# Performance work log

Measured on AMD Instinct MI355X. Metric: run time of the kernel, lower is better.

## Reference

```python
import jax, jax.numpy as jnp
import numpy as np

N_NODES = 50000
N_EDGES = 1600000
D = 64          # n_atom_basis = n_filters
NB = 25         # n_basis (RBF)
L = 3           # n_interactions
CUTOFF = 5.0
MAX_Z = 100


def swish(x):
    return x * jax.nn.sigmoid(x)


def setup_inputs() -> dict:
    key = jax.random.key(0)
    ks = jax.random.split(key, 20)
    z = jax.random.randint(ks[0], (N_NODES,), 0, MAX_Z)
    src = jax.random.randint(ks[1], (N_EDGES,), 0, N_NODES)
    dst = jax.random.randint(ks[2], (N_EDGES,), 0, N_NODES)
    rij = jax.random.uniform(ks[3], (N_EDGES,), jnp.float32, 0.3, CUTOFF)
    s = 1.0 / np.sqrt(D)
    emb = jax.random.normal(ks[4], (MAX_Z, D), jnp.float32) * 0.1
    emb = emb.at[0].set(0.0)  # padding_idx=0
    Win = jax.random.normal(ks[5], (L, D, D), jnp.float32) * s
    Wf1 = jax.random.normal(ks[6], (L, NB, D), jnp.float32) * (1.0 / np.sqrt(NB))
    bf1 = jnp.zeros((L, D), jnp.float32)
    Wf2 = jax.random.normal(ks[7], (L, D, D), jnp.float32) * s
    bf2 = jnp.zeros((L, D), jnp.float32)
    Wo1 = jax.random.normal(ks[8], (L, D, D), jnp.float32) * s
    bo1 = jnp.zeros((L, D), jnp.float32)
    Wo2 = jax.random.normal(ks[9], (L, D, D), jnp.float32) * s
    bo2 = jnp.zeros((L, D), jnp.float32)
    gn_alpha = jnp.ones((L, D), jnp.float32)
    gn_gamma = jnp.ones((L, D), jnp.float32)
    gn_beta = jnp.zeros((L, D), jnp.float32)
    return dict(z=z, src=src, dst=dst, rij=rij, emb=emb, Win=Win,
                Wf1=Wf1, bf1=bf1, Wf2=Wf2, bf2=bf2,
                Wo1=Wo1, bo1=bo1, Wo2=Wo2, bo2=bo2,
                gn_alpha=gn_alpha, gn_gamma=gn_gamma, gn_beta=gn_beta)


def reference(z, src, dst, rij, emb, Win, Wf1, bf1, Wf2, bf2,
              Wo1, bo1, Wo2, bo2, gn_alpha, gn_gamma, gn_beta):
    n = z.shape[0]
    # GaussianSmearing(0, cutoff, n_basis)
    offsets = jnp.linspace(0.0, CUTOFF, NB)
    width = offsets[1] - offsets[0]
    coeff = -0.5 / (width * width)
    fij = jnp.exp(coeff * (rij[:, None] - offsets[None, :]) ** 2)  # [E, NB]
    # CosineCutoff
    C = 0.5 * (jnp.cos(rij * (np.pi / CUTOFF)) + 1.0) * (rij < CUTOFF)  # [E]

    feat = emb[z]  # [N, D]
    for l in range(L):
        # cfconv: in2f (no bias), filter MLP gated by cutoff, gather*W, scatter-sum
        x1 = feat @ Win[l]                                            # [N, D]
        W = swish(fij @ Wf1[l] + bf1[l]) @ Wf2[l] + bf2[l]            # [E, D]
        W = W * C[:, None]
        m = x1[src] * W                                               # [E, D]
        agg = jax.ops.segment_sum(m, dst, num_segments=n)             # [N, D]
        # f2out: Dense+swish, Dense; residual
        y = swish(agg @ Wo1[l] + bo1[l]) @ Wo2[l] + bo2[l]
        feat = feat + y
        # GraphNorm over all nodes (single graph)
        mean = feat.mean(axis=0)
        h = feat - gn_alpha[l] * mean
        var = (h * h).mean(axis=0)
        feat = gn_gamma[l] * h * jax.lax.rsqrt(var + 1e-5) + gn_beta[l]

    # softmax readout: per-feature attention over nodes
    w = jax.nn.softmax(feat, axis=0)
    pooled = (w * feat).sum(axis=0)  # [D]
    return feat, pooled
```

## Files before the change

### kernel.cpp

```cpp
#include <hip/hip_runtime.h>
#include <hip/hip_bf16.h>
#include <math.h>

#define D64 64
#define KTAB 4096
#define TROWS (KTAB + 1)
#define CHUNK 8192
#define PARTB 196
#define TABB 387

typedef unsigned int uint4a __attribute__((ext_vector_type(4), aligned(4)));
typedef __attribute__((ext_vector_type(8))) short bf16x8;
typedef __attribute__((ext_vector_type(4))) float f32x4;

__device__ __forceinline__ void atomAddF(float* p, float v) {
  __hip_atomic_fetch_add(p, v, __ATOMIC_RELAXED, __HIP_MEMORY_SCOPE_AGENT);
}
__device__ __forceinline__ float swishf(float x) { return x / (1.0f + expf(-x)); }
__device__ __forceinline__ float bx(unsigned short s) {
  return __uint_as_float((unsigned)s << 16);
}
__device__ __forceinline__ unsigned short f2b(float f) {
  unsigned u = __float_as_uint(f);
  return (unsigned short)((u + 0x7FFFu + ((u >> 16) & 1u)) >> 16);
}

__global__ __launch_bounds__(256) void k_pre(const int* __restrict__ z,
                                             const float* __restrict__ emb,
                                             float* __restrict__ feat,
                                             const float* __restrict__ Win,
                                             const float* __restrict__ Wo1,
                                             const float* __restrict__ Wo2,
                                             unsigned short* __restrict__ Wb,
                                             const int* __restrict__ dst,
                                             int* __restrict__ bcnt,
                                             int total, int nbInit, int E) {
  __shared__ int c[64];
  const int bid = blockIdx.x;
  if (bid < nbInit) {
    int idx = bid * 256 + threadIdx.x;
    if (idx < total) feat[idx] = emb[z[idx >> 6] * D64 + (idx & 63)];
  } else if (bid < nbInit + 18) {
    int idx = (bid - nbInit) * 256 + threadIdx.x;
    if (idx < 3 * 3 * 64 * 8) {
      const int fr = idx & 7;
      const int lane = (idx >> 3) & 63;
      const int m = (idx >> 9) % 3;
      const int l = idx / 1536;
      const int ct = fr >> 1, ks = fr & 1;
      const int cc = ct * 16 + (lane & 15);
      const int k0 = ks * 32 + (lane >> 4) * 8;
      const float* W = (m == 0 ? Win : (m == 1 ? Wo1 : Wo2)) + (size_t)l * D64 * D64;
      unsigned short* o = &Wb[(size_t)((l * 3 + m) * 64 + lane) * 64 + fr * 8];
#pragma unroll
      for (int j = 0; j < 8; ++j) o[j] = f2b(W[(k0 + j) * D64 + cc]);
    }
  } else {
    const int hb = bid - nbInit - 18;
    if (threadIdx.x < 64) c[threadIdx.x] = 0;
    __syncthreads();
    const int step = 256 * 256 * 4;
    for (int i = (hb * 256 + threadIdx.x) * 4; i < E; i += step) {
      if (i + 4 <= E) {
        int4 d = *(const int4*)&dst[i];
        atomicAdd(&c[d.x >> 10], 1);
        atomicAdd(&c[d.y >> 10], 1);
        atomicAdd(&c[d.z >> 10], 1);
        atomicAdd(&c[d.w >> 10], 1);
      } else {
        for (int q = i; q < E; ++q) atomicAdd(&c[dst[q] >> 10], 1);
      }
    }
    __syncthreads();
    if (threadIdx.x < 64 && c[threadIdx.x] > 0)
      atomicAdd(&bcnt[threadIdx.x], c[threadIdx.x]);
  }
}

__global__ void k_scan64(const int* __restrict__ bcnt, int* __restrict__ bbase,
                         int* __restrict__ gcur, float* __restrict__ stats) {
  const int t = threadIdx.x;
  int v = bcnt[t];
  int x = v;
  for (int o = 1; o < 64; o <<= 1) {
    int y = __shfl_up(x, o);
    if (t >= o) x += y;
  }
  bbase[t] = x - v;
  gcur[t * 16] = x - v;
  if (t == 63) bbase[64] = x;
  stats[128 + t] = 1.0f;
  stats[192 + t] = 0.0f;
}

struct PartS {
  uint2 ord[CHUNK];
  int cnt[64], cbase[64], cpos[64], gpos[64];
  int tot;
  unsigned char obk[CHUNK];
};
struct TabS {
  float w1[25 * D64];
  float w2[D64 * D64];
  float rb[16][D64];
};

__global__ __launch_bounds__(1024) void k_ptab(const int* __restrict__ src,
                                               const int* __restrict__ dst,
                                               const float* __restrict__ rij,
                                               int* __restrict__ gcur,
                                               uint2* __restrict__ rec, int E,
                                               const float* __restrict__ Wf1,
                                               const float* __restrict__ bf1,
                                               const float* __restrict__ Wf2,
                                               const float* __restrict__ bf2,
                                               __hip_bfloat16* __restrict__ Tb) {
  __shared__ __align__(16) char smem[sizeof(PartS) > sizeof(TabS) ? sizeof(PartS)
                                                                  : sizeof(TabS)];
  const int tid = threadIdx.x;
  if (blockIdx.x < PARTB) {
    PartS& S = *(PartS*)smem;
    for (int c = blockIdx.x; (size_t)c * CHUNK < (size_t)E; c += PARTB) {
      const int s0 = c * CHUNK;
      if (tid < 64) S.cnt[tid] = 0;
      __syncthreads();
      const int i0 = s0 + tid * 8;
      int dd[8], ss[8];
      float rr[8];
      bool val[8];
      if (i0 + 8 <= E) {
        int4 d0 = *(const int4*)&dst[i0];
        int4 d1 = *(const int4*)&dst[i0 + 4];
        int4 sa = *(const int4*)&src[i0];
        int4 sb2 = *(const int4*)&src[i0 + 4];
        float4 r0 = *(const float4*)&rij[i0];
        float4 r1 = *(const float4*)&rij[i0 + 4];
        dd[0] = d0.x; dd[1] = d0.y; dd[2] = d0.z; dd[3] = d0.w;
        dd[4] = d1.x; dd[5] = d1.y; dd[6] = d1.z; dd[7] = d1.w;
        ss[0] = sa.x; ss[1] = sa.y; ss[2] = sa.z; ss[3] = sa.w;
        ss[4] = sb2.x; ss[5] = sb2.y; ss[6] = sb2.z; ss[7] = sb2.w;
        rr[0] = r0.x; rr[1] = r0.y; rr[2] = r0.z; rr[3] = r0.w;
        rr[4] = r1.x; rr[5] = r1.y; rr[6] = r1.z; rr[7] = r1.w;
#pragma unroll
        for (int q = 0; q < 8; ++q) val[q] = true;
      } else {
#pragma unroll
        for (int q = 0; q < 8; ++q) {
          int i = i0 + q;
          val[q] = (i < E);
          if (val[q]) { dd[q] = dst[i]; ss[q] = src[i]; rr[q] = rij[i]; }
          else { dd[q] = 0; ss[q] = 0; rr[q] = 0.0f; }
        }
      }
      int bk[8];
      unsigned ry[8];
#pragma unroll
      for (int q = 0; q < 8; ++q) {
        bk[q] = dd[q] >> 10;
        int k = (int)(rr[q] * ((float)KTAB * 0.2f) + 0.5f);
        if (k > KTAB) k = KTAB;
        ry[q] = ((unsigned)ss[q] << 16) | (unsigned)k;
        if (val[q]) atomicAdd(&S.cnt[bk[q]], 1);
      }
      __syncthreads();
      if (tid < 64) {
        int v = S.cnt[tid];
        int x = v;
        for (int o = 1; o < 64; o <<= 1) {
          int y = __shfl_up(x, o);
          if (tid >= o) x += y;
        }
        S.cbase[tid] = x - v;
        S.cpos[tid] = x - v;
        if (tid == 63) S.tot = x;
      }
      __syncthreads();
#pragma unroll
      for (int q = 0; q < 8; ++q) {
        if (val[q]) {
          int slot = atomicAdd(&S.cpos[bk[q]], 1);
          S.ord[slot] = make_uint2((unsigned)dd[q], ry[q]);
          S.obk[slot] = (unsigned char)bk[q];
        }
      }
      __syncthreads();
      if (tid < 64 && S.cnt[tid] > 0)
        S.gpos[tid] = atomicAdd(&gcur[tid * 16], S.cnt[tid]);
      __syncthreads();
      const int tot = S.tot;
      for (int t = tid; t < tot; t += 1024) {
        int b2 = S.obk[t];
        rec[S.gpos[b2] + (t - S.cbase[b2])] = S.ord[t];
      }
      __syncthreads();
    }
  } else {
    TabS& T = *(TabS*)smem;
    const int tb = blockIdx.x - PARTB;
    const int lane = tid & 63;
    const int wsl = tid >> 6;
    const int l = tb / 129;
    const int gb = tb % 129;
    for (int i = tid; i < 25 * D64; i += 1024) T.w1[i] = Wf1[l * 25 * D64 + i];
    for (int i = tid; i < D64 * D64; i += 1024) T.w2[i] = Wf2[l * D64 * D64 + i];
    __syncthreads();
    const float bias1 = bf1[l * D64 + lane];
    const float bias2 = bf2[l * D64 + lane];
    const float width = 5.0f / 24.0f;
    const float coeff = -0.5f / (width * width);
    for (int gi = 0; gi < 2; ++gi) {
      const int g = gb * 32 + wsl * 2 + gi;
      if (g >= TROWS) break;
      const float r = (float)g * (5.0f / KTAB);
      float fv = 0.0f;
      if (lane < 25) { float ddv = r - (float)lane * width; fv = expf(coeff * ddv * ddv); }
      T.rb[wsl][lane] = fv;
      float a1 = bias1;
#pragma unroll
      for (int b = 0; b < 25; ++b)
        a1 = fmaf(T.rb[wsl][b], T.w1[b * D64 + lane], a1);
      float sw = swishf(a1);
      T.rb[wsl][lane] = sw;
      float a2 = bias2;
#pragma unroll
      for (int k = 0; k < D64; ++k)
        a2 = fmaf(T.rb[wsl][k], T.w2[k * D64 + lane], a2);
      float C = (r < 5.0f) ? 0.5f * (cosf(r * 0.62831853f) + 1.0f) : 0.0f;
      Tb[(size_t)(l * TROWS + g) * D64 + lane] = __float2bfloat16(a2 * C);
    }
  }
}

__global__ __launch_bounds__(1024) void k_build(const uint2* __restrict__ rec,
                                                const int* __restrict__ bbase,
                                                int* __restrict__ rp,
                                                unsigned* __restrict__ ep, int n) {
  __shared__ int cnt[1024];
  __shared__ int curl[1024];
  const int tid = threadIdx.x;
  const int b = blockIdx.x;
  const int lo = bbase[b], hi = bbase[b + 1];
  cnt[tid] = 0;
  __syncthreads();
  for (int i = lo + tid; i < hi; i += 1024)
    atomicAdd(&cnt[rec[i].x & 1023], 1);
  __syncthreads();
  const int v = cnt[tid];
  for (int o = 1; o < 1024; o <<= 1) {
    int t = (tid >= o) ? cnt[tid - o] : 0;
    __syncthreads();
    cnt[tid] += t;
    __syncthreads();
  }
  const int excl = cnt[tid] - v;
  curl[tid] = excl;
  const int node = (b << 10) + tid;
  if (node <= n) rp[node] = lo + excl;
  __syncthreads();
  for (int i = lo + tid; i < hi; i += 1024) {
    uint2 e = rec[i];
    int pos = lo + atomicAdd(&curl[e.x & 1023], 1);
    ep[pos] = e.y;
  }
}

__global__ __launch_bounds__(256) void k_x1(const float* __restrict__ feat,
                                            const unsigned short* __restrict__ Wb,
                                            const float* __restrict__ stats,
                                            __hip_bfloat16* __restrict__ x1, int n) {
  const int lane = threadIdx.x & 63;
  const int r16 = lane & 15;
  const int kg = lane >> 4;
  unsigned short* __restrict__ x1u = (unsigned short*)x1;
  const unsigned short* wl = Wb + (size_t)lane * 64;
  bf16x8 bw[4][2];
#pragma unroll
  for (int ct = 0; ct < 4; ++ct)
#pragma unroll
    for (int ks = 0; ks < 2; ++ks)
      bw[ct][ks] = *(const bf16x8*)&wl[(ct * 2 + ks) * 8];
  float sca[2][8], sha[2][8];
#pragma unroll
  for (int ks = 0; ks < 2; ++ks) {
    const int k0 = ks * 32 + kg * 8;
#pragma unroll
    for (int j = 0; j < 8; ++j) {
      sca[ks][j] = stats[128 + k0 + j];
      sha[ks][j] = stats[192 + k0 + j];
    }
  }
  const int ntile = (n + 15) >> 4;
  const int wid = (blockIdx.x * blockDim.x + threadIdx.x) >> 6;
  const int nw = (gridDim.x * blockDim.x) >> 6;
  for (int t = wid; t < ntile; t += nw) {
    const int base = t * 16;
    int ra = base + r16; if (ra > n - 1) ra = n - 1;
    bf16x8 a[2];
#pragma unroll
    for (int ks = 0; ks < 2; ++ks) {
      const float* p = &feat[(size_t)ra * D64 + ks * 32 + kg * 8];
      bf16x8 v;
#pragma unroll
      for (int j = 0; j < 8; ++j) v[j] = (short)f2b(fmaf(p[j], sca[ks][j], sha[ks][j]));
      a[ks] = v;
    }
    f32x4 acc[4];
#pragma unroll
    for (int ct = 0; ct < 4; ++ct) {
      f32x4 z = {0.0f, 0.0f, 0.0f, 0.0f};
      z = __builtin_amdgcn_mfma_f32_16x16x32_bf16(a[0], bw[ct][0], z, 0, 0, 0);
      z = __builtin_amdgcn_mfma_f32_16x16x32_bf16(a[1], bw[ct][1], z, 0, 0, 0);
      acc[ct] = z;
    }
#pragma unroll
    for (int ct = 0; ct < 4; ++ct)
#pragma unroll
      for (int r = 0; r < 4; ++r) {
        const int rm = base + kg * 4 + r;
        if (rm < n) x1u[(size_t)rm * D64 + ct * 16 + r16] = f2b(acc[ct][r]);
      }
  }
}

__global__ __launch_bounds__(256) void k_gather(const __hip_bfloat16* __restrict__ x1,
                                                const __hip_bfloat16* __restrict__ Tb,
                                                const unsigned* __restrict__ ep,
                                                const int* __restrict__ rp,
                                                unsigned short* __restrict__ aggb, int n) {
  const int lane = threadIdx.x & 63;
  const int half = lane >> 5;
  const int fl = lane & 31;
  const unsigned short* __restrict__ x1u = (const unsigned short*)x1;
  const unsigned short* __restrict__ Tu = (const unsigned short*)Tb;
  const int wid = (blockIdx.x * blockDim.x + threadIdx.x) >> 6;
  const int nw = (gridDim.x * blockDim.x) >> 6;
  for (int nd = wid; nd < n; nd += nw) {
    const int j0 = rp[nd], j1 = rp[nd + 1];
    float ax0 = 0.0f, ay0 = 0.0f, ax1 = 0.0f, ay1 = 0.0f;
    int j = j0;
    for (; j + 16 <= j1; j += 16) {
      const uint4a ua = *(const uint4a*)(ep + j + 8 * half);
      const uint4a ub = *(const uint4a*)(ep + j + 8 * half + 4);
      const unsigned u[8] = {ua.x, ua.y, ua.z, ua.w, ub.x, ub.y, ub.z, ub.w};
      ushort2 xv[8], tv[8];
#pragma unroll
      for (int q = 0; q < 8; ++q)
        xv[q] = *(const ushort2*)&x1u[(size_t)(u[q] >> 16) * D64 + fl * 2];
#pragma unroll
      for (int q = 0; q < 8; ++q)
        tv[q] = *(const ushort2*)&Tu[(size_t)(u[q] & 0x1FFFu) * D64 + fl * 2];
#pragma unroll
      for (int q = 0; q < 8; ++q) {
        if (q & 1) {
          ax1 = fmaf(bx(xv[q].x), bx(tv[q].x), ax1);
          ay1 = fmaf(bx(xv[q].y), bx(tv[q].y), ay1);
        } else {
          ax0 = fmaf(bx(xv[q].x), bx(tv[q].x), ax0);
          ay0 = fmaf(bx(xv[q].y), bx(tv[q].y), ay0);
        }
      }
    }
    for (; j + 8 <= j1; j += 8) {
      const uint4a uu = *(const uint4a*)(ep + j + 4 * half);
      const unsigned u0 = uu.x, u1 = uu.y, u2 = uu.z, u3 = uu.w;
      const ushort2 xA = *(const ushort2*)&x1u[(size_t)(u0 >> 16) * D64 + fl * 2];
      const ushort2 xB = *(const ushort2*)&x1u[(size_t)(u1 >> 16) * D64 + fl * 2];
      const ushort2 xC = *(const ushort2*)&x1u[(size_t)(u2 >> 16) * D64 + fl * 2];
      const ushort2 xD = *(const ushort2*)&x1u[(size_t)(u3 >> 16) * D64 + fl * 2];
      const ushort2 tA = *(const ushort2*)&Tu[(size_t)(u0 & 0x1FFFu) * D64 + fl * 2];
      const ushort2 tB = *(const ushort2*)&Tu[(size_t)(u1 & 0x1FFFu) * D64 + fl * 2];
      const ushort2 tC = *(const ushort2*)&Tu[(size_t)(u2 & 0x1FFFu) * D64 + fl * 2];
      const ushort2 tD = *(const ushort2*)&Tu[(size_t)(u3 & 0x1FFFu) * D64 + fl * 2];
      ax0 = fmaf(bx(xA.x), bx(tA.x), ax0);
      ay0 = fmaf(bx(xA.y), bx(tA.y), ay0);
      ax1 = fmaf(bx(xB.x), bx(tB.x), ax1);
      ay1 = fmaf(bx(xB.y), bx(tB.y), ay1);
      ax0 = fmaf(bx(xC.x), bx(tC.x), ax0);
      ay0 = fmaf(bx(xC.y), bx(tC.y), ay0);
      ax1 = fmaf(bx(xD.x), bx(tD.x), ax1);
      ay1 = fmaf(bx(xD.y), bx(tD.y), ay1);
    }
    for (; j + 2 <= j1; j += 2) {
      const unsigned u = ep[j + half];
      const ushort2 xr = *(const ushort2*)&x1u[(size_t)(u >> 16) * D64 + fl * 2];
      const ushort2 tw = *(const ushort2*)&Tu[(size_t)(u & 0x1FFFu) * D64 + fl * 2];
      ax0 = fmaf(bx(xr.x), bx(tw.x), ax0);
      ay0 = fmaf(bx(xr.y), bx(tw.y), ay0);
    }
    if (j < j1 && half == 0) {
      const unsigned u = ep[j];
      const ushort2 xr = *(const ushort2*)&x1u[(size_t)(u >> 16) * D64 + fl * 2];
      const ushort2 tw = *(const ushort2*)&Tu[(size_t)(u & 0x1FFFu) * D64 + fl * 2];
      ax0 = fmaf(bx(xr.x), bx(tw.x), ax0);
      ay0 = fmaf(bx(xr.y), bx(tw.y), ay0);
    }
    float ax = ax0 + ax1, ay = ay0 + ay1;
    ax += __shfl_xor(ax, 32);
    ay += __shfl_xor(ay, 32);
    if (half == 0) {
      unsigned pk = ((unsigned)f2b(ay) << 16) | (unsigned)f2b(ax);
      *(unsigned*)&aggb[(size_t)nd * D64 + fl * 2] = pk;
    }
  }
}

__global__ __launch_bounds__(256) void k_out(const unsigned short* __restrict__ aggb,
                                             const unsigned short* __restrict__ Wb1,
                                             const unsigned short* __restrict__ Wb2,
                                             const float* __restrict__ bo1,
                                             const float* __restrict__ bo2,
                                             const float* __restrict__ nstats,
                                             float* __restrict__ feat,
                                             float* __restrict__ part, int n) {
  __shared__ __align__(16) unsigned short tl[4][16 * 72];
  __shared__ float redp[4][128];
  const int lane = threadIdx.x & 63;
  const int wsl = threadIdx.x >> 6;
  const int r16 = lane & 15;
  const int kg = lane >> 4;
  const unsigned short* wl1 = Wb1 + (size_t)lane * 64;
  const unsigned short* wl2 = Wb2 + (size_t)lane * 64;
  bf16x8 bw1[4][2], bw2[4][2];
#pragma unroll
  for (int ct = 0; ct < 4; ++ct)
#pragma unroll
    for (int ks = 0; ks < 2; ++ks) {
      bw1[ct][ks] = *(const bf16x8*)&wl1[(ct * 2 + ks) * 8];
      bw2[ct][ks] = *(const bf16x8*)&wl2[(ct * 2 + ks) * 8];
    }
  float b1c[4], b2c[4], scc[4], shc[4];
#pragma unroll
  for (int ct = 0; ct < 4; ++ct) {
    b1c[ct] = bo1[ct * 16 + r16];
    b2c[ct] = bo2[ct * 16 + r16];
    scc[ct] = nstats[128 + ct * 16 + r16];
    shc[ct] = nstats[192 + ct * 16 + r16];
  }
  float sf[4] = {0, 0, 0, 0}, sf2[4] = {0, 0, 0, 0};
  unsigned short* tw = tl[wsl];
  const int ntile = (n + 15) >> 4;
  const int wid = (blockIdx.x * blockDim.x + threadIdx.x) >> 6;
  const int nw = (gridDim.x * blockDim.x) >> 6;
  for (int t = wid; t < ntile; t += nw) {
    const int base = t * 16;
    int ra = base + r16; if (ra > n - 1) ra = n - 1;
    bf16x8 a1[2];
#pragma unroll
    for (int ks = 0; ks < 2; ++ks)
      a1[ks] = *(const bf16x8*)&aggb[(size_t)ra * D64 + ks * 32 + kg * 8];
    f32x4 acc[4];
#pragma unroll
    for (int ct = 0; ct < 4; ++ct) {
      f32x4 z = {0.0f, 0.0f, 0.0f, 0.0f};
      z = __builtin_amdgcn_mfma_f32_16x16x32_bf16(a1[0], bw1[ct][0], z, 0, 0, 0);
      z = __builtin_amdgcn_mfma_f32_16x16x32_bf16(a1[1], bw1[ct][1], z, 0, 0, 0);
      acc[ct] = z;
    }
#pragma unroll
    for (int ct = 0; ct < 4; ++ct)
#pragma unroll
      for (int r = 0; r < 4; ++r)
        tw[(kg * 4 + r) * 72 + ct * 16 + r16] = f2b(swishf(acc[ct][r] + b1c[ct]));
    bf16x8 a2[2];
#pragma unroll
    for (int ks = 0; ks < 2; ++ks)
      a2[ks] = *(const bf16x8*)&tw[r16 * 72 + ks * 32 + kg * 8];
    f32x4 acc2[4];
#pragma unroll
    for (int ct = 0; ct < 4; ++ct) {
      f32x4 z = {0.0f, 0.0f, 0.0f, 0.0f};
      z = __builtin_amdgcn_mfma_f32_16x16x32_bf16(a2[0], bw2[ct][0], z, 0, 0, 0);
      z = __builtin_amdgcn_mfma_f32_16x16x32_bf16(a2[1], bw2[ct][1], z, 0, 0, 0);
      acc2[ct] = z;
    }
#pragma unroll
    for (int ct = 0; ct < 4; ++ct)
#pragma unroll
      for (int r = 0; r < 4; ++r) {
        const int rm = base + kg * 4 + r;
        if (rm < n) {
          const size_t ix = (size_t)rm * D64 + ct * 16 + r16;
          float fv = fmaf(feat[ix], scc[ct], shc[ct]);
          float fn = fv + acc2[ct][r] + b2c[ct];
          feat[ix] = fn;
          sf[ct] += fn;
          sf2[ct] += fn * fn;
        }
      }
  }
#pragma unroll
  for (int ct = 0; ct < 4; ++ct) {
    sf[ct] += __shfl_xor(sf[ct], 16);
    sf[ct] += __shfl_xor(sf[ct], 32);
    sf2[ct] += __shfl_xor(sf2[ct], 16);
    sf2[ct] += __shfl_xor(sf2[ct], 32);
  }
  if (kg == 0) {
#pragma unroll
    for (int ct = 0; ct < 4; ++ct) {
      redp[wsl][ct * 16 + r16] = sf[ct];
      redp[wsl][64 + ct * 16 + r16] = sf2[ct];
    }
  }
  __syncthreads();
  if (threadIdx.x < 128) {
    float v = redp[0][threadIdx.x] + redp[1][threadIdx.x] +
              redp[2][threadIdx.x] + redp[3][threadIdx.x];
    atomAddF(&part[(blockIdx.x & 63) * 128 + threadIdx.x], v);
  }
}

__global__ void k_nfin(float* __restrict__ part, float* __restrict__ stats,
                       const float* __restrict__ al, const float* __restrict__ ga,
                       const float* __restrict__ be, int n) {
  const int t = threadIdx.x;
  float s = 0.0f;
#pragma unroll 8
  for (int b = 0; b < 64; ++b) s += part[b * 128 + t];
  __shared__ float red[128];
  red[t] = s;
#pragma unroll 8
  for (int b = 0; b < 64; ++b) part[b * 128 + t] = 0.0f;
  __syncthreads();
  if (t < 64) {
    float invN = 1.0f / (float)n;
    float mu = red[t] * invN;
    float ex2 = red[64 + t] * invN;
    float a = al[t];
    float var = ex2 - (2.0f * a - a * a) * mu * mu;
    float sc = ga[t] * rsqrtf(var + 1e-5f);
    stats[128 + t] = sc;
    stats[192 + t] = be[t] - sc * a * mu;
  }
}

__global__ __launch_bounds__(256) void k_pool(float* __restrict__ feat,
                                              const float* __restrict__ stats,
                                              float* __restrict__ part, int n) {
  __shared__ float redp[4][128];
  const int lane = threadIdx.x & 63;
  const int wsl = threadIdx.x >> 6;
  const float sc = stats[128 + lane], sh = stats[192 + lane];
  float s1 = 0.0f, s2 = 0.0f;
  const int wid = (blockIdx.x * blockDim.x + threadIdx.x) >> 6;
  const int nw = (gridDim.x * blockDim.x) >> 6;
  int base = wid * 4;
  const int stride = nw * 4;
  for (; base + 4 <= n; base += stride) {
    float f0 = feat[(size_t)(base + 0) * D64 + lane];
    float f1 = feat[(size_t)(base + 1) * D64 + lane];
    float f2 = feat[(size_t)(base + 2) * D64 + lane];
    float f3 = feat[(size_t)(base + 3) * D64 + lane];
    f0 = fmaf(f0, sc, sh);
    f1 = fmaf(f1, sc, sh);
    f2 = fmaf(f2, sc, sh);
    f3 = fmaf(f3, sc, sh);
    feat[(size_t)(base + 0) * D64 + lane] = f0;
    feat[(size_t)(base + 1) * D64 + lane] = f1;
    feat[(size_t)(base + 2) * D64 + lane] = f2;
    feat[(size_t)(base + 3) * D64 + lane] = f3;
    float e0 = expf(f0 - 20.0f);
    float e1 = expf(f1 - 20.0f);
    float e2 = expf(f2 - 20.0f);
    float e3 = expf(f3 - 20.0f);
    s1 += (e0 + e1) + (e2 + e3);
    s2 += fmaf(f0, e0, f1 * e1) + fmaf(f2, e2, f3 * e3);
  }
  for (int r = base; r < n; ++r) {
    float f = fmaf(feat[(size_t)r * D64 + lane], sc, sh);
    feat[(size_t)r * D64 + lane] = f;
    float e = expf(f - 20.0f);
    s1 += e;
    s2 += f * e;
  }
  redp[wsl][lane] = s1;
  redp[wsl][64 + lane] = s2;
  __syncthreads();
  if (threadIdx.x < 128) {
    float v = redp[0][threadIdx.x] + redp[1][threadIdx.x] +
              redp[2][threadIdx.x] + redp[3][threadIdx.x];
    atomAddF(&part[(blockIdx.x & 63) * 128 + threadIdx.x], v);
  }
}

__global__ void k_pooled(const float* __restrict__ part, float* __restrict__ out) {
  int d = threadIdx.x;
  float s1 = 0.0f, s2 = 0.0f;
#pragma unroll 8
  for (int b = 0; b < 64; ++b) {
    s1 += part[b * 128 + d];
    s2 += part[b * 128 + 64 + d];
  }
  out[d] = s2 / s1;
}

extern "C" void kernel_launch(void* const* d_in, const int* in_sizes, int n_in,
                              void* d_out, int out_size, void* d_ws, size_t ws_size,
                              hipStream_t stream) {
  const int* z = (const int*)d_in[0];
  const int* src = (const int*)d_in[1];
  const int* dst = (const int*)d_in[2];
  const float* rij = (const float*)d_in[3];
  const float* emb = (const float*)d_in[4];
  const float* Win = (const float*)d_in[5];
  const float* Wf1 = (const float*)d_in[6];
  const float* bf1 = (const float*)d_in[7];
  const float* Wf2 = (const float*)d_in[8];
  const float* bf2 = (const float*)d_in[9];
  const float* Wo1 = (const float*)d_in[10];
  const float* bo1 = (const float*)d_in[11];
  const float* Wo2 = (const float*)d_in[12];
  const float* bo2 = (const float*)d_in[13];
  const float* gal = (const float*)d_in[14];
  const float* gga = (const float*)d_in[15];
  const float* gbe = (const float*)d_in[16];
  const int n = in_sizes[0];
  const int E = in_sizes[1];
  (void)n_in; (void)out_size; (void)ws_size;

  float* feat = (float*)d_out;
  float* pooled = feat + (size_t)n * D64;

  char* w = (char*)d_ws;
  size_t off = 0;
  auto take = [&](size_t bytes) {
    size_t o = (off + 255) & ~(size_t)255;
    off = o + bytes;
    return (void*)(w + o);
  };
  __hip_bfloat16* x1 = (__hip_bfloat16*)take((size_t)n * D64 * 2);
  size_t aggrec = ((size_t)n * D64 * 2 > (size_t)E * 8) ? (size_t)n * D64 * 2
                                                        : (size_t)E * 8;
  unsigned short* aggb = (unsigned short*)take(aggrec);
  uint2* rec = (uint2*)aggb;
  float* stats = (float*)take(256 * 4);
  float* part = (float*)take(64 * 128 * 4);
  __hip_bfloat16* Tb = (__hip_bfloat16*)take((size_t)3 * TROWS * D64 * 2);
  unsigned short* Wb = (unsigned short*)take((size_t)9 * 64 * 64 * 2);
  int* rp = (int*)take((size_t)(n + 1) * 4);
  unsigned* ep = (unsigned*)take((size_t)E * 4);
  int* bbase = (int*)take(65 * 4);
  int* gcur = (int*)take(64 * 16 * 4);
  int* bcnt = (int*)take(64 * 4);

  const int total = n * D64;
  const int nbInit = (total + 255) / 256;

  hipMemsetAsync(bcnt, 0, 64 * 4, stream);
  hipMemsetAsync(part, 0, 64 * 128 * 4, stream);
  k_pre<<<nbInit + 18 + 256, 256, 0, stream>>>(z, emb, feat, Win, Wo1, Wo2, Wb,
                                               dst, bcnt, total, nbInit, E);
  k_scan64<<<1, 64, 0, stream>>>(bcnt, bbase, gcur, stats);
  k_ptab<<<PARTB + TABB, 1024, 0, stream>>>(src, dst, rij, gcur, rec, E,
                                            Wf1, bf1, Wf2, bf2, Tb);
  k_build<<<64, 1024, 0, stream>>>(rec, bbase, rp, ep, n);

  for (int l = 0; l < 3; ++l) {
    k_x1<<<784, 256, 0, stream>>>(feat, Wb + (size_t)(l * 3 + 0) * 64 * 64,
                                  stats, x1, n);
    k_gather<<<2048, 256, 0, stream>>>(x1, Tb + (size_t)l * TROWS * D64,
                                       ep, rp, aggb, n);
    k_out<<<784, 256, 0, stream>>>(aggb,
                                   Wb + (size_t)(l * 3 + 1) * 64 * 64,
                                   Wb + (size_t)(l * 3 + 2) * 64 * 64,
                                   bo1 + l * D64, bo2 + l * D64, stats,
                                   feat, part, n);
    k_nfin<<<1, 128, 0, stream>>>(part, stats, gal + l * D64, gga + l * D64, gbe + l * D64, n);
  }

  k_pool<<<1024, 256, 0, stream>>>(feat, stats, part, n);
  k_pooled<<<1, 64, 0, stream>>>(part, pooled);
}
```

Before: 328.7 us.

## Fold tiny scan and norm-finalize kernels into consumer kernels

Removes the single-block k_scan64 and k_nfin launches. Each consumer block now recomputes the 64-bucket prefix scan or the GraphNorm scale and shift from the partial sums. Separate per-layer partial buffers replace the in-place zeroing that k_nfin did. This cuts four kernel launches and their serialization bubbles, at the cost of redundant reductions in every block (784 blocks each read 8192 floats).

Measured after the change: 332.6 us. About the same (+1.2%).

```diff
diff --git a/kernel.cpp b/kernel.cpp
--- a/kernel.cpp
+++ b/kernel.cpp
@@ -23,6 +23,37 @@
 __device__ __forceinline__ unsigned short f2b(float f) {
   unsigned u = __float_as_uint(f);
   return (unsigned short)((u + 0x7FFFu + ((u >> 16) & 1u)) >> 16);
+}
+
+__device__ __forceinline__ void normReduce(const float* __restrict__ partIn,
+                                           const float* __restrict__ al,
+                                           const float* __restrict__ ga,
+                                           const float* __restrict__ be,
+                                           int n, float* sred, float* snorm) {
+  const int t = threadIdx.x;
+  if (partIn == nullptr) {
+    if (t < 64) { snorm[t] = 1.0f; snorm[64 + t] = 0.0f; }
+    __syncthreads();
+    return;
+  }
+  if (t < 128) {
+    float s = 0.0f;
+#pragma unroll 8
+    for (int b = 0; b < 64; ++b) s += partIn[b * 128 + t];
+    sred[t] = s;
+  }
+  __syncthreads();
+  if (t < 64) {
+    float invN = 1.0f / (float)n;
+    float mu = sred[t] * invN;
+    float ex2 = sred[64 + t] * invN;
+    float a = al[t];
+    float var = ex2 - (2.0f * a - a * a) * mu * mu;
+    float sc = ga[t] * rsqrtf(var + 1e-5f);
+    snorm[t] = sc;
+    snorm[64 + t] = be[t] - sc * a * mu;
+  }
+  __syncthreads();
 }
 
 __global__ __launch_bounds__(256) void k_pre(const int* __restrict__ z,
@@ -77,25 +108,9 @@
   }
 }
 
-__global__ void k_scan64(const int* __restrict__ bcnt, int* __restrict__ bbase,
-                         int* __restrict__ gcur, float* __restrict__ stats) {
-  const int t = threadIdx.x;
-  int v = bcnt[t];
-  int x = v;
-  for (int o = 1; o < 64; o <<= 1) {
-    int y = __shfl_up(x, o);
-    if (t >= o) x += y;
-  }
-  bbase[t] = x - v;
-  gcur[t * 16] = x - v;
-  if (t == 63) bbase[64] = x;
-  stats[128 + t] = 1.0f;
-  stats[192 + t] = 0.0f;
-}
-
 struct PartS {
   uint2 ord[CHUNK];
-  int cnt[64], cbase[64], cpos[64], gpos[64];
+  int cnt[64], cbase[64], cpos[64], gpos[64], sbase[64];
   int tot;
   unsigned char obk[CHUNK];
 };
@@ -108,6 +123,7 @@
 __global__ __launch_bounds__(1024) void k_ptab(const int* __restrict__ src,
                                                const int* __restrict__ dst,
                                                const float* __restrict__ rij,
+                                               const int* __restrict__ bcnt,
                                                int* __restrict__ gcur,
                                                uint2* __restrict__ rec, int E,
                                                const float* __restrict__ Wf1,
@@ -120,6 +136,16 @@
   const int tid = threadIdx.x;
   if (blockIdx.x < PARTB) {
     PartS& S = *(PartS*)smem;
+    if (tid < 64) {
+      int v = bcnt[tid];
+      int x = v;
+      for (int o = 1; o < 64; o <<= 1) {
+        int y = __shfl_up(x, o);
+        if (tid >= o) x += y;
+      }
+      S.sbase[tid] = x - v;
+    }
+    __syncthreads();
     for (int c = blockIdx.x; (size_t)c * CHUNK < (size_t)E; c += PARTB) {
       const int s0 = c * CHUNK;
       if (tid < 64) S.cnt[tid] = 0;
@@ -185,7 +211,7 @@
       }
       __syncthreads();
       if (tid < 64 && S.cnt[tid] > 0)
-        S.gpos[tid] = atomicAdd(&gcur[tid * 16], S.cnt[tid]);
+        S.gpos[tid] = S.sbase[tid] + atomicAdd(&gcur[tid * 16], S.cnt[tid]);
       __syncthreads();
       const int tot = S.tot;
       for (int t = tid; t < tot; t += 1024) {
@@ -232,16 +258,27 @@
 }
 
 __global__ __launch_bounds__(1024) void k_build(const uint2* __restrict__ rec,
-                                                const int* __restrict__ bbase,
+                                                const int* __restrict__ bcnt,
                                                 int* __restrict__ rp,
                                                 unsigned* __restrict__ ep, int n) {
   __shared__ int cnt[1024];
   __shared__ int curl[1024];
+  __shared__ int sb2[65];
   const int tid = threadIdx.x;
   const int b = blockIdx.x;
-  const int lo = bbase[b], hi = bbase[b + 1];
+  if (tid < 64) {
+    int v = bcnt[tid];
+    int x = v;
+    for (int o = 1; o < 64; o <<= 1) {
+      int y = __shfl_up(x, o);
+      if (tid >= o) x += y;
+    }
+    sb2[tid] = x - v;
+    if (tid == 63) sb2[64] = x;
+  }
   cnt[tid] = 0;
   __syncthreads();
+  const int lo = sb2[b], hi = sb2[b + 1];
   for (int i = lo + tid; i < hi; i += 1024)
     atomicAdd(&cnt[rec[i].x & 1023], 1);
   __syncthreads();
@@ -266,8 +303,14 @@
 
 __global__ __launch_bounds__(256) void k_x1(const float* __restrict__ feat,
                                             const unsigned short* __restrict__ Wb,
-                                            const float* __restrict__ stats,
+                                            const float* __restrict__ partIn,
+                                            const float* __restrict__ al,
+                                            const float* __restrict__ ga,
+                                            const float* __restrict__ be,
                                             __hip_bfloat16* __restrict__ x1, int n) {
+  __shared__ float sred[128];
+  __shared__ float snorm[128];
+  normReduce(partIn, al, ga, be, n, sred, snorm);
   const int lane = threadIdx.x & 63;
   const int r16 = lane & 15;
   const int kg = lane >> 4;
@@ -285,8 +328,8 @@
     const int k0 = ks * 32 + kg * 8;
 #pragma unroll
     for (int j = 0; j < 8; ++j) {
-      sca[ks][j] = stats[128 + k0 + j];
-      sha[ks][j] = stats[192 + k0 + j];
+      sca[ks][j] = snorm[k0 + j];
+      sha[ks][j] = snorm[64 + k0 + j];
     }
   }
   const int ntile = (n + 15) >> 4;
@@ -409,11 +452,17 @@
                                              const unsigned short* __restrict__ Wb2,
                                              const float* __restrict__ bo1,
                                              const float* __restrict__ bo2,
-                                             const float* __restrict__ nstats,
+                                             const float* __restrict__ partIn,
+                                             const float* __restrict__ al,
+                                             const float* __restrict__ ga,
+                                             const float* __restrict__ be,
                                              float* __restrict__ feat,
-                                             float* __restrict__ part, int n) {
+                                             float* __restrict__ partOut, int n) {
   __shared__ __align__(16) unsigned short tl[4][16 * 72];
   __shared__ float redp[4][128];
+  __shared__ float sred[128];
+  __shared__ float snorm[128];
+  normReduce(partIn, al, ga, be, n, sred, snorm);
   const int lane = threadIdx.x & 63;
   const int wsl = threadIdx.x >> 6;
   const int r16 = lane & 15;
@@ -433,8 +482,8 @@
   for (int ct = 0; ct < 4; ++ct) {
     b1c[ct] = bo1[ct * 16 + r16];
     b2c[ct] = bo2[ct * 16 + r16];
-    scc[ct] = nstats[128 + ct * 16 + r16];
-    shc[ct] = nstats[192 + ct * 16 + r16];
+    scc[ct] = snorm[ct * 16 + r16];
+    shc[ct] = snorm[64 + ct * 16 + r16];
   }
   float sf[4] = {0, 0, 0, 0}, sf2[4] = {0, 0, 0, 0};
   unsigned short* tw = tl[wsl];
@@ -506,41 +555,23 @@
   if (threadIdx.x < 128) {
     float v = redp[0][threadIdx.x] + redp[1][threadIdx.x] +
               redp[2][threadIdx.x] + redp[3][threadIdx.x];
-    atomAddF(&part[(blockIdx.x & 63) * 128 + threadIdx.x], v);
-  }
-}
-
-__global__ void k_nfin(float* __restrict__ part, float* __restrict__ stats,
-                       const float* __restrict__ al, const float* __restrict__ ga,
-                       const float* __restrict__ be, int n) {
-  const int t = threadIdx.x;
-  float s = 0.0f;
-#pragma unroll 8
-  for (int b = 0; b < 64; ++b) s += part[b * 128 + t];
-  __shared__ float red[128];
-  red[t] = s;
-#pragma unroll 8
-  for (int b = 0; b < 64; ++b) part[b * 128 + t] = 0.0f;
-  __syncthreads();
-  if (t < 64) {
-    float invN = 1.0f / (float)n;
-    float mu = red[t] * invN;
-    float ex2 = red[64 + t] * invN;
-    float a = al[t];
-    float var = ex2 - (2.0f * a - a * a) * mu * mu;
-    float sc = ga[t] * rsqrtf(var + 1e-5f);
-    stats[128 + t] = sc;
-    stats[192 + t] = be[t] - sc * a * mu;
+    atomAddF(&partOut[(blockIdx.x & 63) * 128 + threadIdx.x], v);
   }
 }
 
 __global__ __launch_bounds__(256) void k_pool(float* __restrict__ feat,
-                                              const float* __restrict__ stats,
-                                              float* __restrict__ part, int n) {
+                                              const float* __restrict__ partIn,
+                                              const float* __restrict__ al,
+                                              const float* __restrict__ ga,
+                                              const float* __restrict__ be,
+                                              float* __restrict__ partOut, int n) {
   __shared__ float redp[4][128];
+  __shared__ float sred[128];
+  __shared__ float snorm[128];
+  normReduce(partIn, al, ga, be, n, sred, snorm);
   const int lane = threadIdx.x & 63;
   const int wsl = threadIdx.x >> 6;
-  const float sc = stats[128 + lane], sh = stats[192 + lane];
+  const float sc = snorm[lane], sh = snorm[64 + lane];
   float s1 = 0.0f, s2 = 0.0f;
   const int wid = (blockIdx.x * blockDim.x + threadIdx.x) >> 6;
   const int nw = (gridDim.x * blockDim.x) >> 6;
@@ -579,7 +610,7 @@
   if (threadIdx.x < 128) {
     float v = redp[0][threadIdx.x] + redp[1][threadIdx.x] +
               redp[2][threadIdx.x] + redp[3][threadIdx.x];
-    atomAddF(&part[(blockIdx.x & 63) * 128 + threadIdx.x], v);
+    atomAddF(&partOut[(blockIdx.x & 63) * 128 + threadIdx.x], v);
   }
 }
 
@@ -633,41 +664,45 @@
                                                         : (size_t)E * 8;
   unsigned short* aggb = (unsigned short*)take(aggrec);
   uint2* rec = (uint2*)aggb;
-  float* stats = (float*)take(256 * 4);
-  float* part = (float*)take(64 * 128 * 4);
+  float* part = (float*)take(4 * 64 * 128 * 4);
   __hip_bfloat16* Tb = (__hip_bfloat16*)take((size_t)3 * TROWS * D64 * 2);
   unsigned short* Wb = (unsigned short*)take((size_t)9 * 64 * 64 * 2);
   int* rp = (int*)take((size_t)(n + 1) * 4);
   unsigned* ep = (unsigned*)take((size_t)E * 4);
-  int* bbase = (int*)take(65 * 4);
-  int* gcur = (int*)take(64 * 16 * 4);
-  int* bcnt = (int*)take(64 * 4);
+  int* misc = (int*)take((64 + 64 * 16) * 4);
+  int* bcnt = misc;
+  int* gcur = misc + 64;
 
   const int total = n * D64;
   const int nbInit = (total + 255) / 256;
 
-  hipMemsetAsync(bcnt, 0, 64 * 4, stream);
-  hipMemsetAsync(part, 0, 64 * 128 * 4, stream);
+  hipMemsetAsync(misc, 0, (64 + 64 * 16) * 4, stream);
+  hipMemsetAsync(part, 0, 4 * 64 * 128 * 4, stream);
   k_pre<<<nbInit + 18 + 256, 256, 0, stream>>>(z, emb, feat, Win, Wo1, Wo2, Wb,
                                                dst, bcnt, total, nbInit, E);
-  k_scan64<<<1, 64, 0, stream>>>(bcnt, bbase, gcur, stats);
-  k_ptab<<<PARTB + TABB, 1024, 0, stream>>>(src, dst, rij, gcur, rec, E,
+  k_ptab<<<PARTB + TABB, 1024, 0, stream>>>(src, dst, rij, bcnt, gcur, rec, E,
                                             Wf1, bf1, Wf2, bf2, Tb);
-  k_build<<<64, 1024, 0, stream>>>(rec, bbase, rp, ep, n);
+  k_build<<<64, 1024, 0, stream>>>(rec, bcnt, rp, ep, n);
 
   for (int l = 0; l < 3; ++l) {
+    const float* pin = (l == 0) ? nullptr : part + (size_t)(l - 1) * 8192;
+    const float* al = (l == 0) ? nullptr : gal + (l - 1) * D64;
+    const float* ga = (l == 0) ? nullptr : gga + (l - 1) * D64;
+    const float* be = (l == 0) ? nullptr : gbe + (l - 1) * D64;
     k_x1<<<784, 256, 0, stream>>>(feat, Wb + (size_t)(l * 3 + 0) * 64 * 64,
-                                  stats, x1, n);
+                                  pin, al, ga, be, x1, n);
     k_gather<<<2048, 256, 0, stream>>>(x1, Tb + (size_t)l * TROWS * D64,
                                        ep, rp, aggb, n);
     k_out<<<784, 256, 0, stream>>>(aggb,
                                    Wb + (size_t)(l * 3 + 1) * 64 * 64,
                                    Wb + (size_t)(l * 3 + 2) * 64 * 64,
-                                   bo1 + l * D64, bo2 + l * D64, stats,
-                                   feat, part, n);
-    k_nfin<<<1, 128, 0, stream>>>(part, stats, gal + l * D64, gga + l * D64, gbe + l * D64, n);
-  }
-
-  k_pool<<<1024, 256, 0, stream>>>(feat, stats, part, n);
-  k_pooled<<<1, 64, 0, stream>>>(part, pooled);
-}
+                                   bo1 + l * D64, bo2 + l * D64,
+                                   pin, al, ga, be,
+                                   feat, part + (size_t)l * 8192, n);
+  }
+
+  k_pool<<<1024, 256, 0, stream>>>(feat, part + 2 * 8192,
+                                   gal + 2 * D64, gga + 2 * D64, gbe + 2 * D64,
+                                   part + 3 * 8192, n);
+  k_pooled<<<1, 64, 0, stream>>>(part + 3 * 8192, pooled);
+}
```
